# Kernel tuning notes

Hardware: AMD Instinct MI355X
Metric: run time of the kernel (lower is better)

The kernel has to match this reference:

```python
import jax, jax.numpy as jnp
import numpy as np

N = 100000
E = 3200000
G = 64  # number of graphs


def _lin_params(key, fan_in, fan_out):
    k1, k2 = jax.random.split(key)
    bound = 1.0 / np.sqrt(fan_in)
    W = jax.random.uniform(k1, (fan_in, fan_out), jnp.float32, -bound, bound)
    b = jax.random.uniform(k2, (fan_out,), jnp.float32, -bound, bound)
    return W, b


def setup_inputs() -> dict:
    key = jax.random.key(0)
    ks = jax.random.split(key, 12)
    x = jax.random.normal(ks[0], (N, 3), jnp.float32)
    edge_index = jax.random.randint(ks[1], (2, E), 0, N, jnp.int32)
    batch = jnp.sort(jax.random.randint(ks[2], (N,), 0, G, jnp.int32))
    # conv1: in=3, heads=4, out_channels=16, concat=True -> 64
    Wq1, bq1 = _lin_params(ks[3], 3, 64)
    Wk1, bk1 = _lin_params(ks[4], 3, 64)
    Wv1, bv1 = _lin_params(ks[5], 3, 64)
    Ws1, bs1 = _lin_params(ks[6], 3, 64)
    # conv2: in=64, heads=1, out_channels=6, concat=False -> 6
    Wq2, bq2 = _lin_params(ks[7], 64, 6)
    Wk2, bk2 = _lin_params(ks[8], 64, 6)
    Wv2, bv2 = _lin_params(ks[9], 64, 6)
    Ws2, bs2 = _lin_params(ks[10], 64, 6)
    return dict(x=x, edge_index=edge_index, batch=batch,
                Wq1=Wq1, bq1=bq1, Wk1=Wk1, bk1=bk1, Wv1=Wv1, bv1=bv1, Ws1=Ws1, bs1=bs1,
                Wq2=Wq2, bq2=bq2, Wk2=Wk2, bk2=bk2, Wv2=Wv2, bv2=bv2, Ws2=Ws2, bs2=bs2)


def transformer_conv(x, src, dst, Wq, bq, Wk, bk, Wv, bv, Ws, bs, heads, d, concat):
    n = x.shape[0]
    q = (x @ Wq + bq).reshape(n, heads, d)
    k = (x @ Wk + bk).reshape(n, heads, d)
    v = (x @ Wv + bv).reshape(n, heads, d)
    # per-edge attention logits: query at target, key at source  [E, H]
    logits = jnp.einsum('ehd,ehd->eh', q[dst], k[src]) / jnp.sqrt(jnp.float32(d))
    # segment softmax over incoming edges of each target node
    m = jax.ops.segment_max(logits, dst, num_segments=n)          # [N, H]
    a = jnp.exp(logits - m[dst])                                   # [E, H]
    denom = jax.ops.segment_sum(a, dst, num_segments=n)           # [N, H]
    alpha = a / (denom[dst] + 1e-16)
    out = jax.ops.segment_sum(alpha[:, :, None] * v[src], dst, num_segments=n)  # [N,H,d]
    out = out.reshape(n, heads * d) if concat else out.mean(axis=1)
    return out + x @ Ws + bs  # root/skip connection


def reference(x, edge_index, batch,
              Wq1, bq1, Wk1, bk1, Wv1, bv1, Ws1, bs1,
              Wq2, bq2, Wk2, bk2, Wv2, bv2, Ws2, bs2):
    src, dst = edge_index[0], edge_index[1]
    h = transformer_conv(x, src, dst, Wq1, bq1, Wk1, bk1, Wv1, bv1, Ws1, bs1,
                         heads=4, d=16, concat=True)
    h = jax.nn.relu(h)
    # dropout is identity in eval mode
    h = transformer_conv(h, src, dst, Wq2, bq2, Wk2, bk2, Wv2, bv2, Ws2, bs2,
                         heads=1, d=6, concat=False)
    # global mean pool over graphs
    sums = jax.ops.segment_sum(h, batch, num_segments=G)
    cnts = jax.ops.segment_sum(jnp.ones((h.shape[0],), h.dtype), batch, num_segments=G)
    pooled = sums / jnp.maximum(cnts, 1.0)[:, None]
    return jax.nn.log_softmax(pooled, axis=1)
```

## Files before the change

kernel.cpp:

```cpp
#include <hip/hip_runtime.h>
#include <hip/hip_fp16.h>
#include <math.h>

#define N_NODES 100000
#define N_EDGES 3200000
#define N_GRAPHS 64
#define NEG_INF -1e30f

#define NB 196
#define CAP 18432
#define NBLK 1024
#define CHUNK 3125

__device__ __forceinline__ void atomAddF(float* p, float v) {
#if defined(__HIP_PLATFORM_AMD__)
    unsafeAtomicAdd(p, v);
#else
    atomicAdd(p, v);
#endif
}

__device__ __forceinline__ float b2f(unsigned w, int sh) {
    return (float)(signed char)(w >> sh);
}

__device__ __forceinline__ float kvdot(const float* q, uint4 w, float* sv_out) {
    float2 s = __half22float2(*(const __half2*)&w.w);
    *sv_out = s.y;
    return s.x * (q[0] * b2f(w.x, 0) + q[1] * b2f(w.x, 8)
                + q[2] * b2f(w.x, 16) + q[3] * b2f(w.x, 24)
                + q[4] * b2f(w.y, 0) + q[5] * b2f(w.y, 8));
}

__global__ __launch_bounds__(256) void s1_partition(const int* __restrict__ ei,
                                                    const float* __restrict__ x,
                                                    float4* __restrict__ xp,
                                                    uint2* __restrict__ xh,
                                                    float* __restrict__ psum,
                                                    float* __restrict__ pcnt,
                                                    int* __restrict__ offs,
                                                    unsigned* __restrict__ pairs) {
    __shared__ unsigned pairbuf[CHUNK];
    __shared__ unsigned sortbuf[CHUNK];
    __shared__ unsigned char buckbuf[CHUNK];
    __shared__ int hist[4][200];
    __shared__ int cur[NB], tmp[NB];
    int tid = threadIdx.x;

    {
        int n = blockIdx.x * 98 + tid;
        if (tid < 98 && n < N_NODES) {
            float x0 = x[3 * n], x1 = x[3 * n + 1], x2 = x[3 * n + 2];
            xp[n] = make_float4(x0, x1, x2, 0.f);
            __half2 h01 = __floats2half2_rn(x0, x1);
            __half2 h2p = __floats2half2_rn(x2, 0.f);
            xh[n] = make_uint2(*(unsigned*)&h01, *(unsigned*)&h2p);
        }
    }
    if (blockIdx.x == 0) {
        for (int i = tid; i < N_GRAPHS * 6; i += 256) psum[i] = 0.f;
        for (int i = tid; i < N_GRAPHS; i += 256) pcnt[i] = 0.f;
    }

    int wp = tid >> 6;
    for (int i = tid; i < 4 * 200; i += 256) ((int*)hist)[i] = 0;
    __syncthreads();
    int gbase = blockIdx.x * CHUNK;
    for (int i = tid; i < CHUNK; i += 256) {
        int src = ei[gbase + i];
        unsigned dst = (unsigned)ei[N_EDGES + gbase + i];
        pairbuf[i] = ((unsigned)src << 9) | (dst & 511u);
        unsigned b = dst >> 9;
        buckbuf[i] = (unsigned char)b;
        atomicAdd(&hist[wp][b], 1);
    }
    __syncthreads();
    if (tid < NB) {
        int s = 0;
#pragma unroll
        for (int w = 0; w < 4; ++w) s += hist[w][tid];
        tmp[tid] = s;
        hist[0][tid] = s;
    }
    __syncthreads();
    for (int off = 1; off < NB; off <<= 1) {
        int v = 0;
        if (tid < NB && tid >= off) v = tmp[tid - off];
        __syncthreads();
        if (tid < NB) tmp[tid] += v;
        __syncthreads();
    }
    if (tid < NB) {
        int excl = tmp[tid] - hist[0][tid];
        cur[tid] = excl;
        offs[blockIdx.x * NB + tid] = excl;
    }
    __syncthreads();
    for (int i = tid; i < CHUNK; i += 256) {
        int pos = atomicAdd(&cur[buckbuf[i]], 1);
        sortbuf[pos] = pairbuf[i];
    }
    __syncthreads();
    for (int i = tid; i < CHUNK; i += 256)
        pairs[gbase + i] = sortbuf[i];
}

#define B4T 1024
__global__ __launch_bounds__(B4T) void b4_build(const unsigned* __restrict__ pairs,
                                                const int* __restrict__ offs,
                                                int* __restrict__ rs,
                                                int* __restrict__ re,
                                                int* __restrict__ csr_src) {
    __shared__ unsigned eLDS[CAP];
    __shared__ int so[NBLK], slen[NBLK], dbase[NBLK];
    __shared__ int cnt2[2][512];
    __shared__ int sc[NBLK], cur[512];
    int b = blockIdx.x;
    int tid = threadIdx.x;

    for (int k = tid; k < NBLK; k += B4T) {
        int s = offs[k * NB + b];
        int e = (b == NB - 1) ? CHUNK : offs[k * NB + b + 1];
        so[k] = s;
        slen[k] = e - s;
    }
    ((int*)cnt2)[tid] = 0;
    __syncthreads();
    if (tid < NBLK) sc[tid] = slen[tid];
    __syncthreads();
    for (int off = 1; off < NBLK; off <<= 1) {
        int v = (tid < NBLK && tid >= off) ? sc[tid - off] : 0;
        __syncthreads();
        if (tid < NBLK) sc[tid] += v;
        __syncthreads();
    }
    if (tid < NBLK) dbase[tid] = sc[tid] - slen[tid];
    __syncthreads();
    int ne = dbase[NBLK - 1] + slen[NBLK - 1];

    int sub = tid & 15, sseg = tid >> 4;
    for (int k = sseg; k < NBLK; k += (B4T / 16)) {
        int gb = k * CHUNK + so[k];
        int db = dbase[k], ln = slen[k];
        for (int i = sub; i < ln; i += 16)
            eLDS[db + i] = pairs[gb + i];
    }
    __syncthreads();

    int half = tid >> 9;
    for (int i = tid; i < ne; i += B4T)
        atomicAdd(&cnt2[half][eLDS[i] & 511u], 1);
    __syncthreads();
    int mycnt = 0;
    if (tid < 512) {
        mycnt = cnt2[0][tid] + cnt2[1][tid];
        sc[tid] = mycnt;
    }
    __syncthreads();
    for (int off = 1; off < 512; off <<= 1) {
        int v = (tid < 512 && tid >= off) ? sc[tid - off] : 0;
        __syncthreads();
        if (tid < 512) sc[tid] += v;
        __syncthreads();
    }
    int rbase = b * CAP;
    if (tid < 512) {
        int excl = sc[tid] - mycnt;
        cur[tid] = rbase + excl;
        int node = (b << 9) + tid;
        if (node < N_NODES) {
            rs[node] = rbase + excl;
            re[node] = rbase + sc[tid];
        }
    }
    __syncthreads();
    for (int i = tid; i < ne; i += B4T) {
        unsigned p = eLDS[i];
        int pos = atomicAdd(&cur[p & 511u], 1);
        csr_src[pos] = (int)(p >> 9);
    }
}

__global__ void g1_layer1(const float4* __restrict__ xp,
                          const uint2* __restrict__ xh,
                          const float* __restrict__ Wq, const float* __restrict__ bq,
                          const float* __restrict__ Wk, const float* __restrict__ bk,
                          const float* __restrict__ Wv, const float* __restrict__ bv,
                          const float* __restrict__ Ws, const float* __restrict__ bs,
                          const int* __restrict__ rs, const int* __restrict__ re,
                          const int* __restrict__ csr_src,
                          uint2* __restrict__ h1) {
    __shared__ float sWq[192], sWk[192], sWv[192], sWs[192];
    __shared__ float sbq[64], sbk[64], sbv[64], sbs[64];
    for (int i = threadIdx.x; i < 192; i += 256) {
        sWq[i] = Wq[i]; sWk[i] = Wk[i]; sWv[i] = Wv[i]; sWs[i] = Ws[i];
    }
    for (int i = threadIdx.x; i < 64; i += 256) {
        sbq[i] = bq[i]; sbk[i] = bk[i]; sbv[i] = bv[i]; sbs[i] = bs[i];
    }
    __syncthreads();

    int lane = threadIdx.x & 63;
    int u = lane & 15;
    int slot = u >> 2;
    int j0 = u * 4;
    int n = blockIdx.x * 16 + (threadIdx.x >> 6) * 4 + (lane >> 4);

    float4 xc = xp[n];
    float x0 = xc.x, x1 = xc.y, x2 = xc.z;

    float q[4];
#pragma unroll
    for (int i = 0; i < 4; ++i)
        q[i] = 0.25f * (sbq[j0 + i] + x0 * sWq[j0 + i] + x1 * sWq[64 + j0 + i]
                        + x2 * sWq[128 + j0 + i]);
    float t0 = 0.f, t1 = 0.f, t2 = 0.f, tb = 0.f;
#pragma unroll
    for (int i = 0; i < 4; ++i) {
        float qi = q[i];
        t0 += qi * sWk[j0 + i];
        t1 += qi * sWk[64 + j0 + i];
        t2 += qi * sWk[128 + j0 + i];
        tb += qi * sbk[j0 + i];
    }
#pragma unroll
    for (int off = 1; off <= 2; off <<= 1) {
        t0 += __shfl_xor(t0, off);
        t1 += __shfl_xor(t1, off);
        t2 += __shfl_xor(t2, off);
        tb += __shfl_xor(tb, off);
    }
    int tsrc = (lane & 48) | ((lane & 3) << 2) | ((lane >> 2) & 3);
    t0 = __shfl(t0, tsrc, 64);
    t1 = __shfl(t1, tsrc, 64);
    t2 = __shfl(t2, tsrc, 64);
    tb = __shfl(tb, tsrc, 64);

    int row = rs[n];
    int deg = re[n] - row;

    float m4[4], d4[4], s04[4], s14[4], s24[4];
#pragma unroll
    for (int k = 0; k < 4; ++k) { m4[k] = NEG_INF; d4[k] = 0.f; s04[k] = 0.f; s14[k] = 0.f; s24[k] = 0.f; }
    for (int base = 0; base < deg; base += 16) {
        int src4[4];
        bool v4[4];
#pragma unroll
        for (int k = 0; k < 4; ++k) {
            int e = base + k * 4 + slot;
            v4[k] = e < deg;
            src4[k] = v4[k] ? csr_src[row + e] : 0;
        }
        uint2 w4[4];
#pragma unroll
        for (int k = 0; k < 4; ++k) w4[k] = xh[src4[k]];
#pragma unroll
        for (int k = 0; k < 4; ++k) {
            float2 a01 = __half22float2(*(const __half2*)&w4[k].x);
            float a2 = __half22float2(*(const __half2*)&w4[k].y).x;
            float l = v4[k] ? (tb + a01.x * t0 + a01.y * t1 + a2 * t2) : NEG_INF;
            float mn = fmaxf(m4[k], l);
            float sc = __expf(m4[k] - mn);
            float a = v4[k] ? __expf(l - mn) : 0.f;
            d4[k] = d4[k] * sc + a;
            s04[k] = s04[k] * sc + a * a01.x;
            s14[k] = s14[k] * sc + a * a01.y;
            s24[k] = s24[k] * sc + a * a2;
            m4[k] = mn;
        }
    }
    float m, d, s0, s1, s2;
    {
        float mAB = fmaxf(m4[0], m4[1]);
        float fa = __expf(m4[0] - mAB), fb = __expf(m4[1] - mAB);
        float dAB = d4[0] * fa + d4[1] * fb;
        float s0AB = s04[0] * fa + s04[1] * fb;
        float s1AB = s14[0] * fa + s14[1] * fb;
        float s2AB = s24[0] * fa + s24[1] * fb;
        float mCD = fmaxf(m4[2], m4[3]);
        float fc = __expf(m4[2] - mCD), fd = __expf(m4[3] - mCD);
        float dCD = d4[2] * fc + d4[3] * fd;
        float s0CD = s04[2] * fc + s04[3] * fd;
        float s1CD = s14[2] * fc + s14[3] * fd;
        float s2CD = s24[2] * fc + s24[3] * fd;
        m = fmaxf(mAB, mCD);
        float f1 = __expf(mAB - m), f2 = __expf(mCD - m);
        d = dAB * f1 + dCD * f2;
        s0 = s0AB * f1 + s0CD * f2;
        s1 = s1AB * f1 + s1CD * f2;
        s2 = s2AB * f1 + s2CD * f2;
    }

    float gm = m;
    gm = fmaxf(gm, __shfl_xor(gm, 4));
    gm = fmaxf(gm, __shfl_xor(gm, 8));
    float f = __expf(m - gm);
    d *= f; s0 *= f; s1 *= f; s2 *= f;
#pragma unroll
    for (int off = 4; off <= 8; off <<= 1) {
        d += __shfl_xor(d, off);
        s0 += __shfl_xor(s0, off);
        s1 += __shfl_xor(s1, off);
        s2 += __shfl_xor(s2, off);
    }

    int esrc = (lane & 48) | ((lane >> 2) & 3);
    float dH = __shfl(d, esrc, 64);
    float s0H = __shfl(s0, esrc, 64);
    float s1H = __shfl(s1, esrc, 64);
    float s2H = __shfl(s2, esrc, 64);
    float inv = 1.f / (dH + 1e-16f);
    float fr = dH * inv, r0 = s0H * inv, r1 = s1H * inv, r2 = s2H * inv;

    float o[4];
#pragma unroll
    for (int i = 0; i < 4; ++i) {
        int j = j0 + i;
        float val = fr * sbv[j] + r0 * sWv[j] + r1 * sWv[64 + j] + r2 * sWv[128 + j]
                  + sbs[j] + x0 * sWs[j] + x1 * sWs[64 + j] + x2 * sWs[128 + j];
        o[i] = fmaxf(val, 0.f);
    }
    __half2 p01 = __floats2half2_rn(o[0], o[1]);
    __half2 p23 = __floats2half2_rn(o[2], o[3]);
    h1[(size_t)n * 16 + u] = make_uint2(*(unsigned*)&p01, *(unsigned*)&p23);
}

__global__ void k5_node2(const unsigned* __restrict__ h1,
                         const float* __restrict__ Wq, const float* __restrict__ bq,
                         const float* __restrict__ Wk, const float* __restrict__ bk,
                         const float* __restrict__ Wv, const float* __restrict__ bv,
                         const float* __restrict__ Ws, const float* __restrict__ bs,
                         uint4* __restrict__ q2h, float* __restrict__ s2,
                         uint4* __restrict__ kv2) {
    __shared__ float sWq[384], sWk[384], sWv[384], sWs[384];
    __shared__ float sbq[6], sbk[6], sbv[6], sbs[6];
    for (int i = threadIdx.x; i < 384; i += blockDim.x) {
        sWq[i] = Wq[i]; sWk[i] = Wk[i]; sWv[i] = Wv[i]; sWs[i] = Ws[i];
    }
    if (threadIdx.x < 6) {
        sbq[threadIdx.x] = bq[threadIdx.x];
        sbk[threadIdx.x] = bk[threadIdx.x];
        sbv[threadIdx.x] = bv[threadIdx.x];
        sbs[threadIdx.x] = bs[threadIdx.x];
    }
    __syncthreads();
    int n = blockIdx.x * blockDim.x + threadIdx.x;
    if (n >= N_NODES) return;
    float qa[6], ka[6], va[6], sa[6];
#pragma unroll
    for (int c = 0; c < 6; ++c) { qa[c] = sbq[c]; ka[c] = sbk[c]; va[c] = sbv[c]; sa[c] = sbs[c]; }
    const uint4* hp = reinterpret_cast<const uint4*>(h1 + (size_t)n * 32);
#pragma unroll
    for (int i4 = 0; i4 < 8; ++i4) {
        uint4 hv = hp[i4];
        float2 f01 = __half22float2(*(const __half2*)&hv.x);
        float2 f23 = __half22float2(*(const __half2*)&hv.y);
        float2 f45 = __half22float2(*(const __half2*)&hv.z);
        float2 f67 = __half22float2(*(const __half2*)&hv.w);
        float hvv[8] = {f01.x, f01.y, f23.x, f23.y, f45.x, f45.y, f67.x, f67.y};
#pragma unroll
        for (int uu = 0; uu < 8; ++uu) {
            float hx = hvv[uu];
            int i = i4 * 8 + uu;
#pragma unroll
            for (int c = 0; c < 6; ++c) {
                qa[c] += hx * sWq[i * 6 + c];
                ka[c] += hx * sWk[i * 6 + c];
                va[c] += hx * sWv[i * 6 + c];
                sa[c] += hx * sWs[i * 6 + c];
            }
        }
    }
    const float rsqrt6 = 0.4082482904638631f;
    {
        __half2 h01 = __floats2half2_rn(qa[0] * rsqrt6, qa[1] * rsqrt6);
        __half2 h23 = __floats2half2_rn(qa[2] * rsqrt6, qa[3] * rsqrt6);
        __half2 h45 = __floats2half2_rn(qa[4] * rsqrt6, qa[5] * rsqrt6);
        uint4 w;
        w.x = *(unsigned*)&h01; w.y = *(unsigned*)&h23;
        w.z = *(unsigned*)&h45; w.w = 0u;
        q2h[n] = w;
    }
#pragma unroll
    for (int c = 0; c < 6; ++c) s2[(size_t)n * 6 + c] = sa[c];
    float mk = 0.f, mv = 0.f;
#pragma unroll
    for (int c = 0; c < 6; ++c) {
        mk = fmaxf(mk, fabsf(ka[c]));
        mv = fmaxf(mv, fabsf(va[c]));
    }
    float sk = fmaxf(mk, 1e-8f) * (1.f / 127.f);
    float sv = fmaxf(mv, 1e-8f) * (1.f / 127.f);
    float isk = 1.f / sk, isv = 1.f / sv;
    int qk[6], qv[6];
#pragma unroll
    for (int c = 0; c < 6; ++c) {
        qk[c] = __float2int_rn(ka[c] * isk);
        qv[c] = __float2int_rn(va[c] * isv);
    }
    uint4 w;
    w.x = (qk[0] & 255) | ((qk[1] & 255) << 8) | ((qk[2] & 255) << 16) | ((qk[3] & 255) << 24);
    w.y = (qk[4] & 255) | ((qk[5] & 255) << 8) | ((qv[0] & 255) << 16) | ((qv[1] & 255) << 24);
    w.z = (qv[2] & 255) | ((qv[3] & 255) << 8) | ((qv[4] & 255) << 16) | ((qv[5] & 255) << 24);
    __half2 hs = __floats2half2_rn(sk, sv);
    w.w = *(unsigned*)&hs;
    kv2[n] = w;
}

__global__ void g2_layer2(const int* __restrict__ rs, const int* __restrict__ re,
                          const int* __restrict__ csr_src,
                          const uint4* __restrict__ q2h,
                          const uint4* __restrict__ kv2,
                          const float* __restrict__ s2,
                          const int* __restrict__ batch,
                          float* __restrict__ psum, float* __restrict__ pcnt) {
    __shared__ float bsum[N_GRAPHS * 6];
    __shared__ float bcnt[N_GRAPHS];
    for (int i = threadIdx.x; i < N_GRAPHS * 6; i += 256) bsum[i] = 0.f;
    for (int i = threadIdx.x; i < N_GRAPHS; i += 256) bcnt[i] = 0.f;
    __syncthreads();

    int node = blockIdx.x * 32 + (threadIdx.x >> 3);
    int lane8 = threadIdx.x & 7;

    uint4 qw = q2h[node];
    float2 q01 = __half22float2(*(const __half2*)&qw.x);
    float2 q23 = __half22float2(*(const __half2*)&qw.y);
    float2 q45 = __half22float2(*(const __half2*)&qw.z);
    float q[6] = {q01.x, q01.y, q23.x, q23.y, q45.x, q45.y};
    int row = rs[node];
    int deg = re[node] - row;

    float lg[8], svr[8];
    unsigned py[8], pz[8];
#pragma unroll
    for (int i = 0; i < 8; ++i) { lg[i] = NEG_INF; svr[i] = 0.f; py[i] = 0u; pz[i] = 0u; }
    float lmax = NEG_INF;
    {
        int src4[4];
        bool v4[4];
#pragma unroll
        for (int i = 0; i < 4; ++i) {
            int e = lane8 + i * 8;
            v4[i] = e < deg;
            src4[i] = v4[i] ? csr_src[row + e] : 0;
        }
        uint4 w4[4];
#pragma unroll
        for (int i = 0; i < 4; ++i) w4[i] = kv2[src4[i]];
#pragma unroll
        for (int i = 0; i < 4; ++i) {
            float svx;
            float l = kvdot(q, w4[i], &svx);
            if (v4[i]) {
                lg[i] = l; svr[i] = svx; py[i] = w4[i].y; pz[i] = w4[i].z;
                lmax = fmaxf(lmax, l);
            }
        }
    }
    if (deg > 32) {
        int src4[4];
        bool v4[4];
#pragma unroll
        for (int i = 0; i < 4; ++i) {
            int e = lane8 + (i + 4) * 8;
            v4[i] = e < deg;
            src4[i] = v4[i] ? csr_src[row + e] : 0;
        }
        uint4 w4[4];
#pragma unroll
        for (int i = 0; i < 4; ++i) w4[i] = kv2[src4[i]];
#pragma unroll
        for (int i = 0; i < 4; ++i) {
            float svx;
            float l = kvdot(q, w4[i], &svx);
            if (v4[i]) {
                lg[i + 4] = l; svr[i + 4] = svx; py[i + 4] = w4[i].y; pz[i + 4] = w4[i].z;
                lmax = fmaxf(lmax, l);
            }
        }
    }
    float mo = NEG_INF, dov = 0.f;
    float ao[6] = {0.f, 0.f, 0.f, 0.f, 0.f, 0.f};
    for (int e = lane8 + 64; e < deg; e += 8) {
        int src = csr_src[row + e];
        uint4 w = kv2[src];
        float svx;
        float l = kvdot(q, w, &svx);
        float mn = fmaxf(mo, l);
        float scp = __expf(mo - mn);
        float wx = __expf(l - mn);
        float wsx = wx * svx;
        dov = dov * scp + wx;
        ao[0] = ao[0] * scp + wsx * b2f(w.y, 16);
        ao[1] = ao[1] * scp + wsx * b2f(w.y, 24);
        ao[2] = ao[2] * scp + wsx * b2f(w.z, 0);
        ao[3] = ao[3] * scp + wsx * b2f(w.z, 8);
        ao[4] = ao[4] * scp + wsx * b2f(w.z, 16);
        ao[5] = ao[5] * scp + wsx * b2f(w.z, 24);
        mo = mn;
    }
    lmax = fmaxf(lmax, mo);
    lmax = fmaxf(lmax, __shfl_xor(lmax, 1));
    lmax = fmaxf(lmax, __shfl_xor(lmax, 2));
    lmax = fmaxf(lmax, __shfl_xor(lmax, 4));
    if (lmax < -5e29f) lmax = 0.f;

    float d = 0.f;
    float acc[6] = {0.f, 0.f, 0.f, 0.f, 0.f, 0.f};
#pragma unroll
    for (int i = 0; i < 8; ++i) {
        float w = __expf(lg[i] - lmax);
        float ws = w * svr[i];
        d += w;
        acc[0] += ws * b2f(py[i], 16);
        acc[1] += ws * b2f(py[i], 24);
        acc[2] += ws * b2f(pz[i], 0);
        acc[3] += ws * b2f(pz[i], 8);
        acc[4] += ws * b2f(pz[i], 16);
        acc[5] += ws * b2f(pz[i], 24);
    }
    float so = __expf(mo - lmax);
    d += dov * so;
#pragma unroll
    for (int c = 0; c < 6; ++c) acc[c] += ao[c] * so;

#pragma unroll
    for (int off = 1; off <= 4; off <<= 1) {
        d += __shfl_xor(d, off);
#pragma unroll
        for (int c = 0; c < 6; ++c) acc[c] += __shfl_xor(acc[c], off);
    }

    if (lane8 == 0) {
        float inv = 1.f / (d + 1e-16f);
        int g = batch[node];
#pragma unroll
        for (int c = 0; c < 6; ++c) {
            float val = acc[c] * inv + s2[(size_t)node * 6 + c];
            atomicAdd(&bsum[g * 6 + c], val);
        }
        atomicAdd(&bcnt[g], 1.f);
    }
    __syncthreads();
    for (int i = threadIdx.x; i < N_GRAPHS * 6; i += 256) {
        float v = bsum[i];
        if (v != 0.f) atomAddF(psum + i, v);
    }
    for (int i = threadIdx.x; i < N_GRAPHS; i += 256) {
        float v = bcnt[i];
        if (v != 0.f) atomAddF(pcnt + i, v);
    }
}

__global__ void k9_final(const float* __restrict__ psum, const float* __restrict__ pcnt,
                         float* __restrict__ out) {
    int g = threadIdx.x;
    if (g >= N_GRAPHS) return;
    float cnt = fmaxf(pcnt[g], 1.0f);
    float z[6];
    float mx = -1e30f;
#pragma unroll
    for (int c = 0; c < 6; ++c) {
        z[c] = psum[g * 6 + c] / cnt;
        mx = fmaxf(mx, z[c]);
    }
    float se = 0.f;
#pragma unroll
    for (int c = 0; c < 6; ++c) se += __expf(z[c] - mx);
    float lse = mx + logf(se);
#pragma unroll
    for (int c = 0; c < 6; ++c) out[g * 6 + c] = z[c] - lse;
}

extern "C" void kernel_launch(void* const* d_in, const int* in_sizes, int n_in,
                              void* d_out, int out_size, void* d_ws, size_t ws_size,
                              hipStream_t stream) {
    const float* x   = (const float*)d_in[0];
    const int*   ei  = (const int*)d_in[1];
    const int*   bat = (const int*)d_in[2];
    const float* Wq1 = (const float*)d_in[3];  const float* bq1 = (const float*)d_in[4];
    const float* Wk1 = (const float*)d_in[5];  const float* bk1 = (const float*)d_in[6];
    const float* Wv1 = (const float*)d_in[7];  const float* bv1 = (const float*)d_in[8];
    const float* Ws1 = (const float*)d_in[9];  const float* bs1 = (const float*)d_in[10];
    const float* Wq2 = (const float*)d_in[11]; const float* bq2 = (const float*)d_in[12];
    const float* Wk2 = (const float*)d_in[13]; const float* bk2 = (const float*)d_in[14];
    const float* Wv2 = (const float*)d_in[15]; const float* bv2 = (const float*)d_in[16];
    const float* Ws2 = (const float*)d_in[17]; const float* bs2 = (const float*)d_in[18];
    float* out = (float*)d_out;

    char* ws = (char*)d_ws;
    size_t off = 0;
    auto alloc = [&](size_t bytes) -> char* {
        char* p = ws + off;
        off += (bytes + 255) & ~(size_t)255;
        return p;
    };

    float*    psum    = (float*)   alloc((size_t)N_GRAPHS * 6 * 4);
    float*    pcnt    = (float*)   alloc((size_t)N_GRAPHS * 4);
    int*      offs    = (int*)     alloc((size_t)NBLK * NB * 4);
    unsigned* pairs   = (unsigned*)alloc((size_t)N_EDGES * 4);
    int*      csr_src = (int*)     alloc((size_t)NB * CAP * 4);
    int*      rsv     = (int*)     alloc((size_t)N_NODES * 4);
    int*      rev     = (int*)     alloc((size_t)N_NODES * 4);
    float4*   xp      = (float4*)  alloc((size_t)N_NODES * 16);
    uint2*    xh      = (uint2*)   alloc((size_t)N_NODES * 8);
    unsigned* h1      = (unsigned*)alloc((size_t)N_NODES * 64 * 2);
    uint4*    q2h     = (uint4*)   alloc((size_t)N_NODES * 16);
    float*    s2      = (float*)   alloc((size_t)N_NODES * 6 * 4);
    uint4*    kv2     = (uint4*)   alloc((size_t)N_NODES * 16);

    s1_partition<<<NBLK, 256, 0, stream>>>(ei, x, xp, xh, psum, pcnt, offs, pairs);
    b4_build<<<NB, B4T, 0, stream>>>(pairs, offs, rsv, rev, csr_src);

    g1_layer1<<<N_NODES / 16, 256, 0, stream>>>(xp, xh, Wq1, bq1, Wk1, bk1, Wv1, bv1,
                                                Ws1, bs1, rsv, rev, csr_src,
                                                (uint2*)h1);
    k5_node2<<<(N_NODES + 255) / 256, 256, 0, stream>>>(h1, Wq2, bq2, Wk2, bk2,
                                                        Wv2, bv2, Ws2, bs2,
                                                        q2h, s2, kv2);
    g2_layer2<<<N_NODES / 32, 256, 0, stream>>>(rsv, rev, csr_src, q2h, kv2, s2,
                                                bat, psum, pcnt);
    k9_final<<<1, 64, 0, stream>>>(psum, pcnt, out);
}
```

Before: 136.1 us.

## Fuse layer-2 node projections into layer-1 aggregation kernel via LDS staging

The separate k5_node2 kernel is merged into the layer-1 kernel. Layer-1 outputs are staged in a padded LDS buffer and the four 64x6 projections are computed cooperatively, with 16 threads per node split by matrix and input quarter and combined by shuffle reduction. This removes the fp16 h1 round trip through global memory and one kernel launch. In exchange it adds a block barrier, more LDS per block (possibly lowering occupancy), and divergent tail writes. h1 also stays in fp32 rather than being rounded to fp16.

```diff
diff --git a/kernel.cpp b/kernel.cpp
--- a/kernel.cpp
+++ b/kernel.cpp
@@ -181,22 +181,43 @@
     }
 }
 
-__global__ void g1_layer1(const float4* __restrict__ xp,
-                          const uint2* __restrict__ xh,
-                          const float* __restrict__ Wq, const float* __restrict__ bq,
-                          const float* __restrict__ Wk, const float* __restrict__ bk,
-                          const float* __restrict__ Wv, const float* __restrict__ bv,
-                          const float* __restrict__ Ws, const float* __restrict__ bs,
-                          const int* __restrict__ rs, const int* __restrict__ re,
-                          const int* __restrict__ csr_src,
-                          uint2* __restrict__ h1) {
+__global__ void g1_fused(const float4* __restrict__ xp,
+                         const uint2* __restrict__ xh,
+                         const float* __restrict__ Wq, const float* __restrict__ bq,
+                         const float* __restrict__ Wk, const float* __restrict__ bk,
+                         const float* __restrict__ Wv, const float* __restrict__ bv,
+                         const float* __restrict__ Ws, const float* __restrict__ bs,
+                         const float* __restrict__ Wq2, const float* __restrict__ bq2,
+                         const float* __restrict__ Wk2, const float* __restrict__ bk2,
+                         const float* __restrict__ Wv2, const float* __restrict__ bv2,
+                         const float* __restrict__ Ws2, const float* __restrict__ bs2,
+                         const int* __restrict__ rs, const int* __restrict__ re,
+                         const int* __restrict__ csr_src,
+                         uint4* __restrict__ q2h, float* __restrict__ s2,
+                         uint4* __restrict__ kv2) {
     __shared__ float sWq[192], sWk[192], sWv[192], sWs[192];
     __shared__ float sbq[64], sbk[64], sbv[64], sbs[64];
+    __shared__ float sW2[4][457];
+    __shared__ float sb2[4][6];
+    __shared__ float hbuf[16][65];
     for (int i = threadIdx.x; i < 192; i += 256) {
         sWq[i] = Wq[i]; sWk[i] = Wk[i]; sWv[i] = Wv[i]; sWs[i] = Ws[i];
     }
     for (int i = threadIdx.x; i < 64; i += 256) {
         sbq[i] = bq[i]; sbk[i] = bk[i]; sbv[i] = bv[i]; sbs[i] = bs[i];
+    }
+    for (int idx = threadIdx.x; idx < 384; idx += 256) {
+        int i = idx / 6, c = idx - i * 6;
+        sW2[0][i * 7 + c] = Wq2[idx];
+        sW2[1][i * 7 + c] = Wk2[idx];
+        sW2[2][i * 7 + c] = Wv2[idx];
+        sW2[3][i * 7 + c] = Ws2[idx];
+    }
+    if (threadIdx.x < 6) {
+        sb2[0][threadIdx.x] = bq2[threadIdx.x];
+        sb2[1][threadIdx.x] = bk2[threadIdx.x];
+        sb2[2][threadIdx.x] = bv2[threadIdx.x];
+        sb2[3][threadIdx.x] = bs2[threadIdx.x];
     }
     __syncthreads();
 
@@ -204,7 +225,8 @@
     int u = lane & 15;
     int slot = u >> 2;
     int j0 = u * 4;
-    int n = blockIdx.x * 16 + (threadIdx.x >> 6) * 4 + (lane >> 4);
+    int nl = (threadIdx.x >> 6) * 4 + (lane >> 4);
+    int n = blockIdx.x * 16 + nl;
 
     float4 xc = xp[n];
     float x0 = xc.x, x1 = xc.y, x2 = xc.z;
@@ -269,7 +291,7 @@
             m4[k] = mn;
         }
     }
-    float m, d, s0, s1, s2;
+    float m, d, s0, s1, s2v;
     {
         float mAB = fmaxf(m4[0], m4[1]);
         float fa = __expf(m4[0] - mAB), fb = __expf(m4[1] - mAB);
@@ -288,123 +310,107 @@
         d = dAB * f1 + dCD * f2;
         s0 = s0AB * f1 + s0CD * f2;
         s1 = s1AB * f1 + s1CD * f2;
-        s2 = s2AB * f1 + s2CD * f2;
+        s2v = s2AB * f1 + s2CD * f2;
     }
 
     float gm = m;
     gm = fmaxf(gm, __shfl_xor(gm, 4));
     gm = fmaxf(gm, __shfl_xor(gm, 8));
     float f = __expf(m - gm);
-    d *= f; s0 *= f; s1 *= f; s2 *= f;
+    d *= f; s0 *= f; s1 *= f; s2v *= f;
 #pragma unroll
     for (int off = 4; off <= 8; off <<= 1) {
         d += __shfl_xor(d, off);
         s0 += __shfl_xor(s0, off);
         s1 += __shfl_xor(s1, off);
-        s2 += __shfl_xor(s2, off);
+        s2v += __shfl_xor(s2v, off);
     }
 
     int esrc = (lane & 48) | ((lane >> 2) & 3);
     float dH = __shfl(d, esrc, 64);
     float s0H = __shfl(s0, esrc, 64);
     float s1H = __shfl(s1, esrc, 64);
-    float s2H = __shfl(s2, esrc, 64);
+    float s2H = __shfl(s2v, esrc, 64);
     float inv = 1.f / (dH + 1e-16f);
     float fr = dH * inv, r0 = s0H * inv, r1 = s1H * inv, r2 = s2H * inv;
 
-    float o[4];
 #pragma unroll
     for (int i = 0; i < 4; ++i) {
         int j = j0 + i;
         float val = fr * sbv[j] + r0 * sWv[j] + r1 * sWv[64 + j] + r2 * sWv[128 + j]
                   + sbs[j] + x0 * sWs[j] + x1 * sWs[64 + j] + x2 * sWs[128 + j];
-        o[i] = fmaxf(val, 0.f);
-    }
-    __half2 p01 = __floats2half2_rn(o[0], o[1]);
-    __half2 p23 = __floats2half2_rn(o[2], o[3]);
-    h1[(size_t)n * 16 + u] = make_uint2(*(unsigned*)&p01, *(unsigned*)&p23);
-}
-
-__global__ void k5_node2(const unsigned* __restrict__ h1,
-                         const float* __restrict__ Wq, const float* __restrict__ bq,
-                         const float* __restrict__ Wk, const float* __restrict__ bk,
-                         const float* __restrict__ Wv, const float* __restrict__ bv,
-                         const float* __restrict__ Ws, const float* __restrict__ bs,
-                         uint4* __restrict__ q2h, float* __restrict__ s2,
-                         uint4* __restrict__ kv2) {
-    __shared__ float sWq[384], sWk[384], sWv[384], sWs[384];
-    __shared__ float sbq[6], sbk[6], sbv[6], sbs[6];
-    for (int i = threadIdx.x; i < 384; i += blockDim.x) {
-        sWq[i] = Wq[i]; sWk[i] = Wk[i]; sWv[i] = Wv[i]; sWs[i] = Ws[i];
-    }
-    if (threadIdx.x < 6) {
-        sbq[threadIdx.x] = bq[threadIdx.x];
-        sbk[threadIdx.x] = bk[threadIdx.x];
-        sbv[threadIdx.x] = bv[threadIdx.x];
-        sbs[threadIdx.x] = bs[threadIdx.x];
-    }
-    __syncthreads();
-    int n = blockIdx.x * blockDim.x + threadIdx.x;
-    if (n >= N_NODES) return;
-    float qa[6], ka[6], va[6], sa[6];
-#pragma unroll
-    for (int c = 0; c < 6; ++c) { qa[c] = sbq[c]; ka[c] = sbk[c]; va[c] = sbv[c]; sa[c] = sbs[c]; }
-    const uint4* hp = reinterpret_cast<const uint4*>(h1 + (size_t)n * 32);
-#pragma unroll
-    for (int i4 = 0; i4 < 8; ++i4) {
-        uint4 hv = hp[i4];
-        float2 f01 = __half22float2(*(const __half2*)&hv.x);
-        float2 f23 = __half22float2(*(const __half2*)&hv.y);
-        float2 f45 = __half22float2(*(const __half2*)&hv.z);
-        float2 f67 = __half22float2(*(const __half2*)&hv.w);
-        float hvv[8] = {f01.x, f01.y, f23.x, f23.y, f45.x, f45.y, f67.x, f67.y};
-#pragma unroll
-        for (int uu = 0; uu < 8; ++uu) {
-            float hx = hvv[uu];
-            int i = i4 * 8 + uu;
+        hbuf[nl][j] = fmaxf(val, 0.f);
+    }
+    __syncthreads();
+
+    int t = threadIdx.x;
+    int node_l = t >> 4;
+    int mtx = (t >> 2) & 3;
+    int quarter = t & 3;
+    const float* W2 = sW2[mtx];
+    float p[6] = {0.f, 0.f, 0.f, 0.f, 0.f, 0.f};
+#pragma unroll
+    for (int io = 0; io < 16; ++io) {
+        int i = quarter * 16 + io;
+        float hx = hbuf[node_l][i];
+        int ib = i * 7;
+#pragma unroll
+        for (int c = 0; c < 6; ++c) p[c] += hx * W2[ib + c];
+    }
+#pragma unroll
+    for (int off = 1; off <= 2; off <<= 1) {
+#pragma unroll
+        for (int c = 0; c < 6; ++c) p[c] += __shfl_xor(p[c], off);
+    }
+    float vv[6];
+#pragma unroll
+    for (int c = 0; c < 6; ++c) vv[c] = __shfl(p[c], (lane & 48) | 8, 64);
+
+    int n2 = blockIdx.x * 16 + node_l;
+    const float rsqrt6 = 0.4082482904638631f;
+    if (quarter == 0) {
+        if (mtx == 0) {
+            __half2 h01 = __floats2half2_rn((p[0] + sb2[0][0]) * rsqrt6, (p[1] + sb2[0][1]) * rsqrt6);
+            __half2 h23 = __floats2half2_rn((p[2] + sb2[0][2]) * rsqrt6, (p[3] + sb2[0][3]) * rsqrt6);
+            __half2 h45 = __floats2half2_rn((p[4] + sb2[0][4]) * rsqrt6, (p[5] + sb2[0][5]) * rsqrt6);
+            uint4 w;
+            w.x = *(unsigned*)&h01; w.y = *(unsigned*)&h23;
+            w.z = *(unsigned*)&h45; w.w = 0u;
+            q2h[n2] = w;
+        } else if (mtx == 3) {
+#pragma unroll
+            for (int c = 0; c < 6; ++c) s2[(size_t)n2 * 6 + c] = p[c] + sb2[3][c];
+        } else if (mtx == 1) {
+            float ka[6], va[6];
 #pragma unroll
             for (int c = 0; c < 6; ++c) {
-                qa[c] += hx * sWq[i * 6 + c];
-                ka[c] += hx * sWk[i * 6 + c];
-                va[c] += hx * sWv[i * 6 + c];
-                sa[c] += hx * sWs[i * 6 + c];
+                ka[c] = p[c] + sb2[1][c];
+                va[c] = vv[c] + sb2[2][c];
             }
-        }
-    }
-    const float rsqrt6 = 0.4082482904638631f;
-    {
-        __half2 h01 = __floats2half2_rn(qa[0] * rsqrt6, qa[1] * rsqrt6);
-        __half2 h23 = __floats2half2_rn(qa[2] * rsqrt6, qa[3] * rsqrt6);
-        __half2 h45 = __floats2half2_rn(qa[4] * rsqrt6, qa[5] * rsqrt6);
-        uint4 w;
-        w.x = *(unsigned*)&h01; w.y = *(unsigned*)&h23;
-        w.z = *(unsigned*)&h45; w.w = 0u;
-        q2h[n] = w;
-    }
-#pragma unroll
-    for (int c = 0; c < 6; ++c) s2[(size_t)n * 6 + c] = sa[c];
-    float mk = 0.f, mv = 0.f;
-#pragma unroll
-    for (int c = 0; c < 6; ++c) {
-        mk = fmaxf(mk, fabsf(ka[c]));
-        mv = fmaxf(mv, fabsf(va[c]));
-    }
-    float sk = fmaxf(mk, 1e-8f) * (1.f / 127.f);
-    float sv = fmaxf(mv, 1e-8f) * (1.f / 127.f);
-    float isk = 1.f / sk, isv = 1.f / sv;
-    int qk[6], qv[6];
-#pragma unroll
-    for (int c = 0; c < 6; ++c) {
-        qk[c] = __float2int_rn(ka[c] * isk);
-        qv[c] = __float2int_rn(va[c] * isv);
-    }
-    uint4 w;
-    w.x = (qk[0] & 255) | ((qk[1] & 255) << 8) | ((qk[2] & 255) << 16) | ((qk[3] & 255) << 24);
-    w.y = (qk[4] & 255) | ((qk[5] & 255) << 8) | ((qv[0] & 255) << 16) | ((qv[1] & 255) << 24);
-    w.z = (qv[2] & 255) | ((qv[3] & 255) << 8) | ((qv[4] & 255) << 16) | ((qv[5] & 255) << 24);
-    __half2 hs = __floats2half2_rn(sk, sv);
-    w.w = *(unsigned*)&hs;
-    kv2[n] = w;
+            float mk = 0.f, mv = 0.f;
+#pragma unroll
+            for (int c = 0; c < 6; ++c) {
+                mk = fmaxf(mk, fabsf(ka[c]));
+                mv = fmaxf(mv, fabsf(va[c]));
+            }
+            float sk = fmaxf(mk, 1e-8f) * (1.f / 127.f);
+            float sv = fmaxf(mv, 1e-8f) * (1.f / 127.f);
+            float isk = 1.f / sk, isv = 1.f / sv;
+            int qk[6], qv[6];
+#pragma unroll
+            for (int c = 0; c < 6; ++c) {
+                qk[c] = __float2int_rn(ka[c] * isk);
+                qv[c] = __float2int_rn(va[c] * isv);
+            }
+            uint4 w;
+            w.x = (qk[0] & 255) | ((qk[1] & 255) << 8) | ((qk[2] & 255) << 16) | ((qk[3] & 255) << 24);
+            w.y = (qk[4] & 255) | ((qk[5] & 255) << 8) | ((qv[0] & 255) << 16) | ((qv[1] & 255) << 24);
+            w.z = (qv[2] & 255) | ((qv[3] & 255) << 8) | ((qv[4] & 255) << 16) | ((qv[5] & 255) << 24);
+            __half2 hs = __floats2half2_rn(sk, sv);
+            w.w = *(unsigned*)&hs;
+            kv2[n2] = w;
+        }
+    }
 }
 
 __global__ void g2_layer2(const int* __restrict__ rs, const int* __restrict__ re,
@@ -606,7 +612,6 @@
     int*      rev     = (int*)     alloc((size_t)N_NODES * 4);
     float4*   xp      = (float4*)  alloc((size_t)N_NODES * 16);
     uint2*    xh      = (uint2*)   alloc((size_t)N_NODES * 8);
-    unsigned* h1      = (unsigned*)alloc((size_t)N_NODES * 64 * 2);
     uint4*    q2h     = (uint4*)   alloc((size_t)N_NODES * 16);
     float*    s2      = (float*)   alloc((size_t)N_NODES * 6 * 4);
     uint4*    kv2     = (uint4*)   alloc((size_t)N_NODES * 16);
@@ -614,12 +619,10 @@
     s1_partition<<<NBLK, 256, 0, stream>>>(ei, x, xp, xh, psum, pcnt, offs, pairs);
     b4_build<<<NB, B4T, 0, stream>>>(pairs, offs, rsv, rev, csr_src);
 
-    g1_layer1<<<N_NODES / 16, 256, 0, stream>>>(xp, xh, Wq1, bq1, Wk1, bk1, Wv1, bv1,
-                                                Ws1, bs1, rsv, rev, csr_src,
-                                                (uint2*)h1);
-    k5_node2<<<(N_NODES + 255) / 256, 256, 0, stream>>>(h1, Wq2, bq2, Wk2, bk2,
-                                                        Wv2, bv2, Ws2, bs2,
-                                                        q2h, s2, kv2);
+    g1_fused<<<N_NODES / 16, 256, 0, stream>>>(xp, xh, Wq1, bq1, Wk1, bk1, Wv1, bv1,
+                                               Ws1, bs1, Wq2, bq2, Wk2, bk2,
+                                               Wv2, bv2, Ws2, bs2,
+                                               rsv, rev, csr_src, q2h, s2, kv2);
     g2_layer2<<<N_NODES / 32, 256, 0, stream>>>(rsv, rev, csr_src, q2h, kv2, s2,
                                                 bat, psum, pcnt);
     k9_final<<<1, 64, 0, stream>>>(psum, pcnt, out);
```

Result: slower. 143.5 us (+5.4%).
